# Performance work log

Measured on AMD Instinct MI355X. Metric: run time of the kernel, lower is better.

## Reference

```python
import jax, jax.numpy as jnp
import numpy as np
import math

B, N, DIM = 4, 2048, 512
HEADS, DIM_HEAD = 8, 64
INNER = HEADS * DIM_HEAD  # 512


def setup_inputs() -> dict:
    key = jax.random.key(0)
    ks = jax.random.split(key, 4)
    x = jax.random.normal(ks[0], (B, N, DIM), dtype=jnp.float32)
    # nn.Linear(dim, inner*4, bias=False): store as [dim, 4*inner] for x @ W
    w_qkvg = jax.random.normal(ks[1], (DIM, 4 * INNER), dtype=jnp.float32) * (1.0 / math.sqrt(DIM))
    sigma = jnp.full((1, HEADS, 1, 1), 1.92, dtype=jnp.float32)
    w_out = jax.random.normal(ks[2], (2 * INNER, DIM), dtype=jnp.float32) * (1.0 / math.sqrt(2 * INNER))
    b_out = jax.random.normal(ks[3], (DIM,), dtype=jnp.float32) * 0.01
    return {"x": x, "w_qkvg": w_qkvg, "sigma": sigma, "w_out": w_out, "b_out": b_out}


def reference(x, w_qkvg, sigma, w_out, b_out):
    b, n, d = x.shape
    h, dh = HEADS, DIM_HEAD
    scale = dh ** (-0.5)

    qkvg = x @ w_qkvg  # [b, n, 4*inner]
    q, k, vg, vsigma = jnp.split(qkvg, 4, axis=-1)

    def to_heads(t):  # [b, n, h*dh] -> [b, h, n, dh]
        return t.reshape(b, n, h, dh).transpose(0, 2, 1, 3)

    q, k, vg, vsigma = map(to_heads, (q, k, vg, vsigma))

    # --- softmax branch ---
    dots = jnp.einsum('bhid,bhjd->bhij', q, k) * scale  # [b, h, n, n]
    corr_g = jax.nn.softmax(dots, axis=-1)
    out_g = jnp.matmul(corr_g, vg)  # [b, h, n, dh]

    # --- Gaussian positional-mask branch ---
    pos = jnp.arange(1, n + 1, dtype=x.dtype)
    diffs = jnp.abs(pos[:, None] - pos[None, :])  # [n, n]
    inv_norm = 1.0 / (jnp.sqrt(jnp.asarray(2.0 * math.pi, x.dtype)) * sigma)  # [1, h, 1, 1]
    gm = inv_norm * jnp.exp(-(diffs ** 2)[None, None] / (2.0 * sigma ** 2))  # [1, h, n, n]
    corr_sigma = gm / gm.sum(-1, keepdims=True)
    out_s = jnp.matmul(corr_sigma, vsigma)  # broadcasts over batch -> [b, h, n, dh]

    out = jnp.concatenate([out_g, out_s], axis=-1)  # [b, h, n, 2*dh]
    out = out.transpose(0, 2, 1, 3).reshape(b, n, 2 * h * dh)
    return out @ w_out + b_out
```

## Files before the change

### kernel.cpp

```cpp
#include <hip/hip_runtime.h>

typedef _Float16 f16;
typedef __attribute__((ext_vector_type(8))) _Float16 f16x8;
typedef __attribute__((ext_vector_type(4))) _Float16 f16x4;
typedef __attribute__((ext_vector_type(4))) float f32x4;

#define B_ 4
#define N_ 2048
#define DIM_ 512
#define H_ 8
#define DH_ 64

__device__ __forceinline__ void gload16(const void* g, void* l) {
    __builtin_amdgcn_global_load_lds((const __attribute__((address_space(1))) void*)g,
                                     (__attribute__((address_space(3))) void*)l, 16, 0, 0);
}


__global__ __launch_bounds__(256) void cvt_f16_k8(const float* __restrict__ in,
                                                  f16* __restrict__ out, int n8) {
    int i = blockIdx.x * 256 + threadIdx.x;
    if (i < n8) {
        const float4 a = ((const float4*)in)[i * 2];
        const float4 b = ((const float4*)in)[i * 2 + 1];
        f16x8 o = {(f16)a.x, (f16)a.y, (f16)a.z, (f16)a.w,
                   (f16)b.x, (f16)b.y, (f16)b.z, (f16)b.w};
        ((f16x8*)out)[i] = o;
    }
}

__global__ __launch_bounds__(256) void transpose_cvt_k(const float* __restrict__ in,
                                                       f16* __restrict__ out, int K, int N) {
    __shared__ f16 tile[64][72];
    const int nbk = K >> 6;
    const int bk = blockIdx.x % nbk, bn = blockIdx.x / nbk;
    const int k0 = bk << 6, n0 = bn << 6;
    const int t = threadIdx.x;
    const int r = t >> 2, q = (t & 3) << 4;
#pragma unroll
    for (int u = 0; u < 4; u++) {
        const float4 v = *(const float4*)&in[(size_t)(k0 + r) * N + n0 + q + u * 4];
        tile[q + u * 4 + 0][r] = (f16)v.x;
        tile[q + u * 4 + 1][r] = (f16)v.y;
        tile[q + u * 4 + 2][r] = (f16)v.z;
        tile[q + u * 4 + 3][r] = (f16)v.w;
    }
    __syncthreads();
#pragma unroll
    for (int u = 0; u < 2; u++) {
        f16x8 o = *(const f16x8*)&tile[r][q + u * 8];
        *(f16x8*)&out[(size_t)(n0 + r) * K + k0 + q + u * 8] = o;
    }
}

template <int EPI>
__global__ __launch_bounds__(256) void gemm_bt(
    const f16* __restrict__ A, const f16* __restrict__ BT, int K, int N,
    f16* __restrict__ qb, f16* __restrict__ kb, f16* __restrict__ vbT,
    f16* __restrict__ vs16, const float* __restrict__ bias, float* __restrict__ outp)
{
    __shared__ char sAb[16384];
    __shared__ char sBb[16384];
    const int tid = threadIdx.x;
    const int m0 = blockIdx.y * 128, n0 = blockIdx.x * 128;
    const int wave = tid >> 6, lane = tid & 63;
    const int wr = wave >> 1, wc = wave & 1;
    const int lr = lane & 15, lg = lane >> 4;

    f32x4 acc[4][4];
    const f32x4 zero = {0.f, 0.f, 0.f, 0.f};
#pragma unroll
    for (int i = 0; i < 4; i++)
#pragma unroll
        for (int j = 0; j < 4; j++) acc[i][j] = zero;

    const f16* srcA[4]; const f16* srcB[4];
    char* ldsA[4]; char* ldsB[4];
#pragma unroll
    for (int u = 0; u < 4; u++) {
        int row = wave * 8 + u * 32 + (lane >> 3);
        int e0 = ((lane & 7) ^ (row & 7)) << 3;
        srcA[u] = A + (size_t)(m0 + row) * K + e0;
        srcB[u] = BT + (size_t)(n0 + row) * K + e0;
        ldsA[u] = sAb + wave * 1024 + u * 4096;
        ldsB[u] = sBb + wave * 1024 + u * 4096;
    }

    const int swz = (lr & 7) << 4;
    for (int kt = 0; kt < K; kt += 64) {
#pragma unroll
        for (int u = 0; u < 4; u++) {
            gload16(srcA[u], ldsA[u]);
            gload16(srcB[u], ldsB[u]);
            srcA[u] += 64; srcB[u] += 64;
        }
        __syncthreads();
#pragma unroll
        for (int half = 0; half < 2; half++) {
            f16x8 af[4], bf[4];
#pragma unroll
            for (int i = 0; i < 4; i++) {
                int R = wr * 64 + i * 16 + lr;
                af[i] = *(const f16x8*)(sAb + R * 128 + (((half << 6) | (lg << 4)) ^ swz));
            }
#pragma unroll
            for (int j = 0; j < 4; j++) {
                int R = wc * 64 + j * 16 + lr;
                bf[j] = *(const f16x8*)(sBb + R * 128 + (((half << 6) | (lg << 4)) ^ swz));
            }
#pragma unroll
            for (int i = 0; i < 4; i++)
#pragma unroll
                for (int j = 0; j < 4; j++)
                    acc[i][j] = __builtin_amdgcn_mfma_f32_16x16x32_f16(af[i], bf[j], acc[i][j], 0, 0, 0);
        }
        __syncthreads();
    }

#pragma unroll
    for (int i = 0; i < 4; i++) {
#pragma unroll
        for (int j = 0; j < 4; j++) {
            int col = n0 + wc * 64 + j * 16 + lr;
            int row0 = m0 + wr * 64 + i * 16 + lg * 4;
            if (EPI == 0) {
                int sec = col >> 9, cc = col & 511;
                int h = cc >> 6, d = cc & 63;
                int b = row0 >> 11, ns = row0 & 2047;
                if (sec == 2) {
                    f16x4 o;
#pragma unroll
                    for (int r = 0; r < 4; r++) o[r] = (f16)acc[i][j][r];
                    *(f16x4*)&vbT[((size_t)(b * H_ + h) * DH_ + d) * N_ + ns] = o;
                } else if (sec == 0) {
#pragma unroll
                    for (int r = 0; r < 4; r++)
                        qb[((size_t)(b * H_ + h) * N_ + ns + r) * DH_ + d] = (f16)(acc[i][j][r] * 0.1803368801f);
                } else if (sec == 1) {
#pragma unroll
                    for (int r = 0; r < 4; r++)
                        kb[((size_t)(b * H_ + h) * N_ + ns + r) * DH_ + d] = (f16)acc[i][j][r];
                } else {
#pragma unroll
                    for (int r = 0; r < 4; r++)
                        vs16[((size_t)(b * H_ + h) * N_ + ns + r) * DH_ + d] = (f16)acc[i][j][r];
                }
            } else {
#pragma unroll
                for (int r = 0; r < 4; r++)
                    outp[(size_t)(row0 + r) * N + col] = acc[i][j][r] + bias[col];
            }
        }
    }
}

__global__ __launch_bounds__(256) void gemm_small(
    const f16* __restrict__ A, const f16* __restrict__ BT, int K, int N,
    const float* __restrict__ bias, float* __restrict__ outp)
{
    __shared__ char sAb[8192];
    __shared__ char sBb[8192];
    const int tid = threadIdx.x;
    const int m0 = blockIdx.y * 64, n0 = blockIdx.x * 64;
    const int wave = tid >> 6, lane = tid & 63;
    const int wr = wave >> 1, wc = wave & 1;
    const int lr = lane & 15, lg = lane >> 4;

    f32x4 acc[2][2];
    const f32x4 zero = {0.f, 0.f, 0.f, 0.f};
#pragma unroll
    for (int i = 0; i < 2; i++)
#pragma unroll
        for (int j = 0; j < 2; j++) acc[i][j] = zero;

    const f16* srcA[2]; const f16* srcB[2];
    char* ldsA[2]; char* ldsB[2];
#pragma unroll
    for (int u = 0; u < 2; u++) {
        int row = wave * 8 + u * 32 + (lane >> 3);
        int e0 = ((lane & 7) ^ (row & 7)) << 3;
        srcA[u] = A + (size_t)(m0 + row) * K + e0;
        srcB[u] = BT + (size_t)(n0 + row) * K + e0;
        ldsA[u] = sAb + wave * 1024 + u * 4096;
        ldsB[u] = sBb + wave * 1024 + u * 4096;
    }

    const int swz = (lr & 7) << 4;
    for (int kt = 0; kt < K; kt += 64) {
#pragma unroll
        for (int u = 0; u < 2; u++) {
            gload16(srcA[u], ldsA[u]);
            gload16(srcB[u], ldsB[u]);
            srcA[u] += 64; srcB[u] += 64;
        }
        __syncthreads();
#pragma unroll
        for (int half = 0; half < 2; half++) {
            f16x8 af[2], bf[2];
#pragma unroll
            for (int i = 0; i < 2; i++) {
                int R = wr * 32 + i * 16 + lr;
                af[i] = *(const f16x8*)(sAb + R * 128 + (((half << 6) | (lg << 4)) ^ swz));
            }
#pragma unroll
            for (int j = 0; j < 2; j++) {
                int R = wc * 32 + j * 16 + lr;
                bf[j] = *(const f16x8*)(sBb + R * 128 + (((half << 6) | (lg << 4)) ^ swz));
            }
#pragma unroll
            for (int i = 0; i < 2; i++)
#pragma unroll
                for (int j = 0; j < 2; j++)
                    acc[i][j] = __builtin_amdgcn_mfma_f32_16x16x32_f16(af[i], bf[j], acc[i][j], 0, 0, 0);
        }
        __syncthreads();
    }

#pragma unroll
    for (int i = 0; i < 2; i++)
#pragma unroll
        for (int j = 0; j < 2; j++) {
            int col = n0 + wc * 32 + j * 16 + lr;
            int row0 = m0 + wr * 32 + i * 16 + lg * 4;
#pragma unroll
            for (int r = 0; r < 4; r++)
                outp[(size_t)(row0 + r) * N + col] = acc[i][j][r] + bias[col];
        }
}

__global__ __launch_bounds__(256) void attn_k(
    const f16* __restrict__ qb, const f16* __restrict__ kb, const f16* __restrict__ vbT,
    f16* __restrict__ cat, f16* __restrict__ oaccB, float* __restrict__ lacc)
{
    __shared__ char sKbf[3 * 8192];
    __shared__ char sVbf[2 * 8192];
    const int tid = threadIdx.x;
    const int bid0 = blockIdx.x;
    const int obid = (bid0 & 7) * 128 + (bid0 >> 3);
    const int bh = obid >> 5, qblk = (obid >> 1) & 15, half = obid & 1;
    const int b = bh >> 3, h = bh & 7;
    const int hn = half << 4;
    const int wave = tid >> 6, lane = tid & 63;
    const int lr = lane & 15, lg = lane >> 4;

    const size_t base = (size_t)bh * N_ * DH_;
    const int qrow_a = qblk * 128 + wave * 32 + lr;
    const int qrow_b = qrow_a + 16;
    const f16x8 qfa0 = *(const f16x8*)&qb[base + (size_t)qrow_a * DH_ + lg * 8];
    const f16x8 qfa1 = *(const f16x8*)&qb[base + (size_t)qrow_a * DH_ + 32 + lg * 8];
    const f16x8 qfb0 = *(const f16x8*)&qb[base + (size_t)qrow_b * DH_ + lg * 8];
    const f16x8 qfb1 = *(const f16x8*)&qb[base + (size_t)qrow_b * DH_ + 32 + lg * 8];

    const f16* kq[2]; const f16* vq[2];
#pragma unroll
    for (int u = 0; u < 2; u++) {
        int row = wave * 8 + u * 32 + (lane >> 3);
        int e0 = ((lane & 7) ^ (row & 7)) << 3;
        kq[u] = kb + base + (size_t)row * 64 + e0;
        vq[u] = vbT + base + (size_t)row * 2048 + e0;
    }
    char* const ldsKw = sKbf + wave * 1024;
    char* const ldsVw = sVbf + wave * 1024;

    f32x4 Ota[4], Otb[4], lacc_a, lacc_b;
    const f32x4 zero = {0.f, 0.f, 0.f, 0.f};
#pragma unroll
    for (int dt = 0; dt < 4; dt++) { Ota[dt] = zero; Otb[dt] = zero; }
    lacc_a = zero; lacc_b = zero;
    const f16x8 ones8 = {(f16)1.f, (f16)1.f, (f16)1.f, (f16)1.f,
                         (f16)1.f, (f16)1.f, (f16)1.f, (f16)1.f};

    const int swz = (lr & 7) << 4;

#pragma unroll
    for (int u = 0; u < 2; u++) gload16(kq[u] + (size_t)hn * 4096, ldsKw + u * 4096);
#pragma unroll
    for (int u = 0; u < 2; u++) gload16(vq[u] + hn * 64, ldsVw + u * 4096);
#pragma unroll
    for (int u = 0; u < 2; u++) gload16(kq[u] + (size_t)(hn + 1) * 4096, ldsKw + 8192 + u * 4096);

    int kcur = 0, kpre = 2;
    for (int t = 0; t < 16; t++) {
        __builtin_amdgcn_s_barrier();
        {
            const int vtn = hn + ((t + 1) & 15), ktn = hn + ((t + 2) & 15);
            char* vdst = ldsVw + ((t + 1) & 1) * 8192;
            char* kdst = ldsKw + kpre * 8192;
#pragma unroll
            for (int u = 0; u < 2; u++) gload16(vq[u] + vtn * 64, vdst + u * 4096);
#pragma unroll
            for (int u = 0; u < 2; u++) gload16(kq[u] + (size_t)ktn * 4096, kdst + u * 4096);
        }
        asm volatile("s_waitcnt vmcnt(6)" ::: "memory");
        __builtin_amdgcn_sched_barrier(0);

        const char* Kb = sKbf + kcur * 8192;
        const char* Vb = sVbf + (t & 1) * 8192;

        f32x4 sta[4], stb[4];
        __builtin_amdgcn_s_setprio(1);
#pragma unroll
        for (int ct = 0; ct < 4; ct++) {
            int row = ct * 16 + lr;
            f16x8 kf0 = *(const f16x8*)(Kb + (((row << 7) | (lg << 4)) ^ swz));
            f16x8 kf1 = *(const f16x8*)(Kb + (((row << 7) | 64 | (lg << 4)) ^ swz));
            f32x4 sa = __builtin_amdgcn_mfma_f32_16x16x32_f16(kf0, qfa0, zero, 0, 0, 0);
            sta[ct]  = __builtin_amdgcn_mfma_f32_16x16x32_f16(kf1, qfa1, sa, 0, 0, 0);
            f32x4 sb = __builtin_amdgcn_mfma_f32_16x16x32_f16(kf0, qfb0, zero, 0, 0, 0);
            stb[ct]  = __builtin_amdgcn_mfma_f32_16x16x32_f16(kf1, qfb1, sb, 0, 0, 0);
        }
        __builtin_amdgcn_s_setprio(0);

        f16x4 ppa[4], ppb[4];
#pragma unroll
        for (int ct = 0; ct < 4; ct++)
#pragma unroll
            for (int r = 0; r < 4; r++) {
                ppa[ct][r] = (f16)__builtin_amdgcn_exp2f(sta[ct][r]);
                ppb[ct][r] = (f16)__builtin_amdgcn_exp2f(stb[ct][r]);
            }

        __builtin_amdgcn_s_setprio(1);
#pragma unroll
        for (int c = 0; c < 2; c++) {
            f16x8 bfa = __builtin_shufflevector(ppa[2 * c], ppa[2 * c + 1], 0, 1, 2, 3, 4, 5, 6, 7);
            f16x8 bfb = __builtin_shufflevector(ppb[2 * c], ppb[2 * c + 1], 0, 1, 2, 3, 4, 5, 6, 7);
            lacc_a = __builtin_amdgcn_mfma_f32_16x16x32_f16(ones8, bfa, lacc_a, 0, 0, 0);
            lacc_b = __builtin_amdgcn_mfma_f32_16x16x32_f16(ones8, bfb, lacc_b, 0, 0, 0);
#pragma unroll
            for (int dt = 0; dt < 4; dt++) {
                int row = dt * 16 + lr;
                f16x4 vlo = *(const f16x4*)(Vb + (((row << 7) | (c << 6) | (lg << 3)) ^ swz));
                f16x4 vhi = *(const f16x4*)(Vb + (((row << 7) | (c << 6) | 32 | (lg << 3)) ^ swz));
                f16x8 vf = __builtin_shufflevector(vlo, vhi, 0, 1, 2, 3, 4, 5, 6, 7);
                Ota[dt] = __builtin_amdgcn_mfma_f32_16x16x32_f16(vf, bfa, Ota[dt], 0, 0, 0);
                Otb[dt] = __builtin_amdgcn_mfma_f32_16x16x32_f16(vf, bfb, Otb[dt], 0, 0, 0);
            }
        }
        __builtin_amdgcn_s_setprio(0);

        kcur = (kcur == 2) ? 0 : kcur + 1;
        kpre = (kpre == 2) ? 0 : kpre + 1;
    }

#pragma unroll
    for (int dt = 0; dt < 4; dt++) {
        f16x4 oa, ob;
#pragma unroll
        for (int r = 0; r < 4; r++) {
            oa[r] = (f16)Ota[dt][r];
            ob[r] = (f16)Otb[dt][r];
        }
        if (half == 0) {
            *(f16x4*)&cat[((size_t)(b * N_ + qrow_a)) * 1024 + h * 128 + dt * 16 + lg * 4] = oa;
            *(f16x4*)&cat[((size_t)(b * N_ + qrow_b)) * 1024 + h * 128 + dt * 16 + lg * 4] = ob;
        } else {
            *(f16x4*)&oaccB[((size_t)(bh * N_ + qrow_a)) * 64 + dt * 16 + lg * 4] = oa;
            *(f16x4*)&oaccB[((size_t)(bh * N_ + qrow_b)) * 64 + dt * 16 + lg * 4] = ob;
        }
    }
    if (lg == 0) {
        lacc[half * (32 * N_) + bh * N_ + qrow_a] = lacc_a[0];
        lacc[half * (32 * N_) + bh * N_ + qrow_b] = lacc_b[0];
    }
}

__global__ __launch_bounds__(256) void combine_k(
    f16* __restrict__ cat, const f16* __restrict__ oaccB, const float* __restrict__ lacc)
{
    int gi = blockIdx.x * 256 + threadIdx.x;
    int row = gi >> 3, c8 = gi & 7;
    int bh = row >> 11, q = row & 2047;
    int b = bh >> 3, h = bh & 7;
    float inv = 1.0f / (lacc[row] + lacc[32 * N_ + row]);
    f16* cp = &cat[((size_t)(b * N_ + q)) * 1024 + h * 128 + c8 * 8];
    f16x8 a = *(const f16x8*)cp;
    f16x8 o2 = *(const f16x8*)&oaccB[(size_t)row * 64 + c8 * 8];
    f16x8 o;
#pragma unroll
    for (int i = 0; i < 8; i++) o[i] = (f16)(((float)a[i] + (float)o2[i]) * inv);
    *(f16x8*)cp = o;
}

__global__ __launch_bounds__(256) void gauss_k(
    const f16* __restrict__ vs16, const float* __restrict__ sigma, f16* __restrict__ cat)
{
    const int tid = threadIdx.x;
    const int bh = blockIdx.y, b = bh >> 3, h = bh & 7;
    const int i0 = blockIdx.x * 64;
    const int wv = tid >> 6, d = tid & 63;
    const float sig = sigma[h];
    const float c = 0.72134752f / (sig * sig);

    float wt[17];
#pragma unroll
    for (int o = 0; o <= 16; o++) wt[o] = __builtin_amdgcn_exp2f(-(float)(o * o) * c);
    float wfull = wt[0];
#pragma unroll
    for (int o = 1; o <= 16; o++) wfull += 2.f * wt[o];
    const float inv_wfull = 1.0f / wfull;

    const size_t base = (size_t)bh * N_ * DH_;
    const int r0 = i0 + wv * 16 - 16;
    float v[48];
#pragma unroll
    for (int k = 0; k < 48; k++) {
        int r = r0 + k; r = r < 0 ? 0 : (r > N_ - 1 ? N_ - 1 : r);
        v[k] = (float)vs16[base + (size_t)r * DH_ + d];
    }

#pragma unroll
    for (int it = 0; it < 16; it++) {
        int i = i0 + wv * 16 + it;
        float acc = 0.f;
        if (i >= 16 && i <= N_ - 17) {
#pragma unroll
            for (int o = -16; o <= 16; o++)
                acc += wt[o < 0 ? -o : o] * v[16 + it + o];
            acc *= inv_wfull;
        } else {
            float ws = 0.f;
#pragma unroll
            for (int o = -16; o <= 16; o++) {
                int j = i + o;
                if (j >= 0 && j <= N_ - 1) {
                    float w = wt[o < 0 ? -o : o];
                    ws += w;
                    acc += w * v[16 + it + o];
                }
            }
            acc /= ws;
        }
        cat[((size_t)(b * N_ + i)) * 1024 + h * 128 + 64 + d] = (f16)acc;
    }
}


extern "C" void kernel_launch(void* const* d_in, const int* in_sizes, int n_in,
                              void* d_out, int out_size, void* d_ws, size_t ws_size,
                              hipStream_t stream) {
    const float* x      = (const float*)d_in[0];
    const float* w_qkvg = (const float*)d_in[1];
    const float* sigma  = (const float*)d_in[2];
    const float* w_out  = (const float*)d_in[3];
    const float* b_out  = (const float*)d_in[4];
    float* out = (float*)d_out;
    char* ws = (char*)d_ws;

    const size_t MB = 1048576;
    f16*   x16  = (f16*)(ws);
    float* lacc = (float*)(ws);
    f16*   wqT  = (f16*)(ws + 8 * MB);
    f16*   woT  = (f16*)(ws + 10 * MB);
    f16*   qb   = (f16*)(ws + 11 * MB);
    f16*   kb   = (f16*)(ws + 19 * MB);
    f16*   vbT  = (f16*)(ws + 27 * MB);
    f16*   vs16 = (f16*)(ws + 35 * MB);
    f16*   cat  = (f16*)(ws + 43 * MB);
    f16*   oaccB= (f16*)(ws + 59 * MB);
    if (ws_size < 67 * MB) return;

    cvt_f16_k8<<<2048, 256, 0, stream>>>(x, x16, B_ * N_ * DIM_ / 8);
    transpose_cvt_k<<<256, 256, 0, stream>>>(w_qkvg, wqT, 512, 2048);
    transpose_cvt_k<<<128, 256, 0, stream>>>(w_out, woT, 1024, 512);

    gemm_bt<0><<<dim3(16, 64), 256, 0, stream>>>(x16, wqT, 512, 2048,
                                                 qb, kb, vbT, vs16, nullptr, nullptr);

    attn_k<<<1024, 256, 0, stream>>>(qb, kb, vbT, cat, oaccB, lacc);
    combine_k<<<2048, 256, 0, stream>>>(cat, oaccB, lacc);
    gauss_k<<<dim3(32, 32), 256, 0, stream>>>(vs16, sigma, cat);

    gemm_small<<<dim3(8, 128), 256, 0, stream>>>(cat, woT, 1024, 512, b_out, out);
}
```

Baseline: 130.9 us.

## Remap GEMM blocks for XCD locality and simplify attention K/V double buffering

Both GEMMs now use a 1D grid whose block index is remapped so that blocks on the same XCD share A-row tiles, aiming for better L2 reuse. The attention kernel drops the triple-buffered K prefetch with partial vmcnt waits. It now uses plain double buffering, with a full vmcnt(0) wait and barrier at the end of each iteration. This frees LDS, but the full wait may expose load latency that the deeper pipeline used to hide.

```diff
diff --git a/kernel.cpp b/kernel.cpp
--- a/kernel.cpp
+++ b/kernel.cpp
@@ -53,16 +53,18 @@
     }
 }
 
-template <int EPI>
-__global__ __launch_bounds__(256) void gemm_bt(
+__global__ __launch_bounds__(256) void gemm_bt0(
     const f16* __restrict__ A, const f16* __restrict__ BT, int K, int N,
     f16* __restrict__ qb, f16* __restrict__ kb, f16* __restrict__ vbT,
-    f16* __restrict__ vs16, const float* __restrict__ bias, float* __restrict__ outp)
+    f16* __restrict__ vs16)
 {
     __shared__ char sAb[16384];
     __shared__ char sBb[16384];
     const int tid = threadIdx.x;
-    const int m0 = blockIdx.y * 128, n0 = blockIdx.x * 128;
+    const int bid = blockIdx.x;
+    const int xcd = bid & 7, w = bid >> 3;
+    const int m0 = ((xcd << 3) + (w >> 4)) << 7;
+    const int n0 = (w & 15) << 7;
     const int wave = tid >> 6, lane = tid & 63;
     const int wr = wave >> 1, wc = wave & 1;
     const int lr = lane & 15, lg = lane >> 4;
@@ -123,32 +125,26 @@
         for (int j = 0; j < 4; j++) {
             int col = n0 + wc * 64 + j * 16 + lr;
             int row0 = m0 + wr * 64 + i * 16 + lg * 4;
-            if (EPI == 0) {
-                int sec = col >> 9, cc = col & 511;
-                int h = cc >> 6, d = cc & 63;
-                int b = row0 >> 11, ns = row0 & 2047;
-                if (sec == 2) {
-                    f16x4 o;
-#pragma unroll
-                    for (int r = 0; r < 4; r++) o[r] = (f16)acc[i][j][r];
-                    *(f16x4*)&vbT[((size_t)(b * H_ + h) * DH_ + d) * N_ + ns] = o;
-                } else if (sec == 0) {
-#pragma unroll
-                    for (int r = 0; r < 4; r++)
-                        qb[((size_t)(b * H_ + h) * N_ + ns + r) * DH_ + d] = (f16)(acc[i][j][r] * 0.1803368801f);
-                } else if (sec == 1) {
-#pragma unroll
-                    for (int r = 0; r < 4; r++)
-                        kb[((size_t)(b * H_ + h) * N_ + ns + r) * DH_ + d] = (f16)acc[i][j][r];
-                } else {
-#pragma unroll
-                    for (int r = 0; r < 4; r++)
-                        vs16[((size_t)(b * H_ + h) * N_ + ns + r) * DH_ + d] = (f16)acc[i][j][r];
-                }
+            int sec = col >> 9, cc = col & 511;
+            int h = cc >> 6, d = cc & 63;
+            int b = row0 >> 11, ns = row0 & 2047;
+            if (sec == 2) {
+                f16x4 o;
+#pragma unroll
+                for (int r = 0; r < 4; r++) o[r] = (f16)acc[i][j][r];
+                *(f16x4*)&vbT[((size_t)(b * H_ + h) * DH_ + d) * N_ + ns] = o;
+            } else if (sec == 0) {
+#pragma unroll
+                for (int r = 0; r < 4; r++)
+                    qb[((size_t)(b * H_ + h) * N_ + ns + r) * DH_ + d] = (f16)(acc[i][j][r] * 0.1803368801f);
+            } else if (sec == 1) {
+#pragma unroll
+                for (int r = 0; r < 4; r++)
+                    kb[((size_t)(b * H_ + h) * N_ + ns + r) * DH_ + d] = (f16)acc[i][j][r];
             } else {
 #pragma unroll
                 for (int r = 0; r < 4; r++)
-                    outp[(size_t)(row0 + r) * N + col] = acc[i][j][r] + bias[col];
+                    vs16[((size_t)(b * H_ + h) * N_ + ns + r) * DH_ + d] = (f16)acc[i][j][r];
             }
         }
     }
@@ -161,7 +157,10 @@
     __shared__ char sAb[8192];
     __shared__ char sBb[8192];
     const int tid = threadIdx.x;
-    const int m0 = blockIdx.y * 64, n0 = blockIdx.x * 64;
+    const int bid = blockIdx.x;
+    const int xcd = bid & 7, w = bid >> 3;
+    const int m0 = ((xcd << 4) + (w >> 3)) << 6;
+    const int n0 = (w & 7) << 6;
     const int wave = tid >> 6, lane = tid & 63;
     const int wr = wave >> 1, wc = wave & 1;
     const int lr = lane & 15, lg = lane >> 4;
@@ -232,7 +231,7 @@
     const f16* __restrict__ qb, const f16* __restrict__ kb, const f16* __restrict__ vbT,
     f16* __restrict__ cat, f16* __restrict__ oaccB, float* __restrict__ lacc)
 {
-    __shared__ char sKbf[3 * 8192];
+    __shared__ char sKbf[2 * 8192];
     __shared__ char sVbf[2 * 8192];
     const int tid = threadIdx.x;
     const int bid0 = blockIdx.x;
@@ -276,25 +275,21 @@
     for (int u = 0; u < 2; u++) gload16(kq[u] + (size_t)hn * 4096, ldsKw + u * 4096);
 #pragma unroll
     for (int u = 0; u < 2; u++) gload16(vq[u] + hn * 64, ldsVw + u * 4096);
-#pragma unroll
-    for (int u = 0; u < 2; u++) gload16(kq[u] + (size_t)(hn + 1) * 4096, ldsKw + 8192 + u * 4096);
-
-    int kcur = 0, kpre = 2;
+    asm volatile("s_waitcnt vmcnt(0)" ::: "memory");
+    __builtin_amdgcn_s_barrier();
+
     for (int t = 0; t < 16; t++) {
-        __builtin_amdgcn_s_barrier();
         {
-            const int vtn = hn + ((t + 1) & 15), ktn = hn + ((t + 2) & 15);
+            const int tn = hn + ((t + 1) & 15);
             char* vdst = ldsVw + ((t + 1) & 1) * 8192;
-            char* kdst = ldsKw + kpre * 8192;
-#pragma unroll
-            for (int u = 0; u < 2; u++) gload16(vq[u] + vtn * 64, vdst + u * 4096);
-#pragma unroll
-            for (int u = 0; u < 2; u++) gload16(kq[u] + (size_t)ktn * 4096, kdst + u * 4096);
-        }
-        asm volatile("s_waitcnt vmcnt(6)" ::: "memory");
-        __builtin_amdgcn_sched_barrier(0);
-
-        const char* Kb = sKbf + kcur * 8192;
+            char* kdst = ldsKw + ((t + 1) & 1) * 8192;
+#pragma unroll
+            for (int u = 0; u < 2; u++) gload16(vq[u] + tn * 64, vdst + u * 4096);
+#pragma unroll
+            for (int u = 0; u < 2; u++) gload16(kq[u] + (size_t)tn * 4096, kdst + u * 4096);
+        }
+
+        const char* Kb = sKbf + (t & 1) * 8192;
         const char* Vb = sVbf + (t & 1) * 8192;
 
         f32x4 sta[4], stb[4];
@@ -339,8 +334,8 @@
         }
         __builtin_amdgcn_s_setprio(0);
 
-        kcur = (kcur == 2) ? 0 : kcur + 1;
-        kpre = (kpre == 2) ? 0 : kpre + 1;
+        asm volatile("s_waitcnt vmcnt(0)" ::: "memory");
+        __builtin_amdgcn_s_barrier();
     }
 
 #pragma unroll
@@ -464,12 +459,11 @@
     transpose_cvt_k<<<256, 256, 0, stream>>>(w_qkvg, wqT, 512, 2048);
     transpose_cvt_k<<<128, 256, 0, stream>>>(w_out, woT, 1024, 512);
 
-    gemm_bt<0><<<dim3(16, 64), 256, 0, stream>>>(x16, wqT, 512, 2048,
-                                                 qb, kb, vbT, vs16, nullptr, nullptr);
+    gemm_bt0<<<1024, 256, 0, stream>>>(x16, wqT, 512, 2048, qb, kb, vbT, vs16);
 
     attn_k<<<1024, 256, 0, stream>>>(qb, kb, vbT, cat, oaccB, lacc);
     combine_k<<<2048, 256, 0, stream>>>(cat, oaccB, lacc);
     gauss_k<<<dim3(32, 32), 256, 0, stream>>>(vs16, sigma, cat);
 
-    gemm_small<<<dim3(8, 128), 256, 0, stream>>>(cat, woT, 1024, 512, b_out, out);
-}
+    gemm_small<<<1024, 256, 0, stream>>>(cat, woT, 1024, 512, b_out, out);
+}
```

Result: faster. 122.9 us (-6.1%).
